# Performance work log

Measured on AMD Instinct MI355X. Metric: run time of the kernel, lower is better.

Reference implementation:

```python
import jax, jax.numpy as jnp
from jax import lax
import numpy as np

D = 128      # embedding_dim == GRU input_size == hidden_size
B, S, L = 256, 32, 32  # users, slates per user, slate length


def setup_inputs() -> dict:
    key = jax.random.key(0)
    ks = jax.random.split(key, 8)
    sc = 1.0 / np.sqrt(D)  # PyTorch GRU/Linear init scale
    return {
        "item_embs": jax.random.normal(ks[0], (B, S, L, D), jnp.float32),
        "user_embs": jax.random.normal(ks[1], (B, S, D), jnp.float32),
        "W_ih": jax.random.normal(ks[2], (3 * D, D), jnp.float32) * sc,
        "W_hh": jax.random.normal(ks[3], (3 * D, D), jnp.float32) * sc,
        "b_ih": jax.random.normal(ks[4], (3 * D,), jnp.float32) * sc,
        "b_hh": jax.random.normal(ks[5], (3 * D,), jnp.float32) * sc,
        "W_out": jax.random.normal(ks[6], (1, D), jnp.float32) * sc,
        "b_out": jax.random.normal(ks[7], (1,), jnp.float32) * sc,
    }


def reference(item_embs, user_embs, W_ih, W_hh, b_ih, b_hh, W_out, b_out):
    b, s, l, d = item_embs.shape
    x = item_embs.reshape(b * s, l, d)          # [N, L, D]
    h0 = user_embs.reshape(b * s, d)            # [N, D] initial hidden per slate

    # Precompute input-side gate projections for all timesteps (one big GEMM).
    gx = jnp.einsum('nld,gd->nlg', x, W_ih) + b_ih  # [N, L, 3D], PyTorch gate order r,z,n

    def step(h, gx_t):
        gh = h @ W_hh.T + b_hh                   # [N, 3D]
        xr, xz, xn = jnp.split(gx_t, 3, axis=-1)
        hr, hz, hn = jnp.split(gh, 3, axis=-1)
        r = jax.nn.sigmoid(xr + hr)
        z = jax.nn.sigmoid(xz + hz)
        n = jnp.tanh(xn + r * hn)
        h_new = (1.0 - z) * n + z * h
        return h_new, h_new

    _, hs = lax.scan(step, h0, jnp.swapaxes(gx, 0, 1))  # hs: [L, N, D]
    rnn_out = jnp.swapaxes(hs, 0, 1)             # [N, L, D]
    out = rnn_out @ W_out.T + b_out              # [N, L, 1]
    return out.reshape(b, s, l)
```

## Files before the change

kernel.cpp:

```cpp
#include <hip/hip_runtime.h>
#include <math.h>

#define DD   128
#define LL   32
#define MS   32
#define NT   1024
#define NSEQ 8192
#define XP   136
#define GP   36
#define OLP  36

#define GX_ELEMS   (384 * GP)
#define SMEM_XH_X  (2 * 384 * GP * 4)
#define SMEM_XH_H  (SMEM_XH_X + 2 * MS * XP * 2)
#define SMEM_OUTL  (SMEM_XH_H + 2 * MS * XP * 2)
#define SMEM_WOFL  (SMEM_OUTL + MS * OLP * 4)
#define SMEM_TOTAL (SMEM_WOFL + 4 * 64 * 8 * 2)

typedef short bf16x8 __attribute__((ext_vector_type(8)));
typedef float f32x4  __attribute__((ext_vector_type(4)));

#define MFMA __builtin_amdgcn_mfma_f32_16x16x32_bf16

__device__ __forceinline__ unsigned short f2bf(float f) {
    unsigned u = __float_as_uint(f);
    u += 0x7fffu + ((u >> 16) & 1u);
    return (unsigned short)(u >> 16);
}

#if __has_builtin(__builtin_amdgcn_cvt_pk_bf16_f32)
typedef __bf16 bf16x2_t __attribute__((ext_vector_type(2)));
__device__ __forceinline__ unsigned pack2(float a, float b) {
    union { bf16x2_t v; unsigned u; } c;
    c.v = __builtin_amdgcn_cvt_pk_bf16_f32(a, b);
    return c.u;
}
#else
__device__ __forceinline__ unsigned pack2(float a, float b) {
    return (unsigned)f2bf(a) | ((unsigned)f2bf(b) << 16);
}
#endif

__device__ __forceinline__ void pack8(float4 a, float4 b, unsigned short* dst) {
    union { unsigned u[4]; bf16x8 v; } pk;
    pk.u[0] = pack2(a.x, a.y); pk.u[1] = pack2(a.z, a.w);
    pk.u[2] = pack2(b.x, b.y); pk.u[3] = pack2(b.z, b.w);
    *(bf16x8*)dst = pk.v;
}

__device__ __forceinline__ float fast_rcp(float x) {
    return __builtin_amdgcn_rcpf(x);
}

__global__ void prep_weights(const float* __restrict__ Wih,
                             const float* __restrict__ Whh,
                             unsigned short* __restrict__ Wfrag) {
    int idx  = blockIdx.x * blockDim.x + threadIdx.x;
    int j    = idx & 7;
    int lane = (idx >> 3) & 63;
    int kk   = (idx >> 9) & 3;
    int sl   = (idx >> 11) & 7;
    int sg   = idx >> 14;
    int n = lane & 15, q = lane >> 4;
    int k  = kk * 32 + q * 8 + j;
    int g  = (sg >= 3) ? sg - 3 : sg;
    int gd = g * 128 + sl * 16 + n;
    const float* src = (sg >= 3) ? Whh : Wih;
    Wfrag[idx] = f2bf(src[gd * 128 + k]);
}

__global__ __launch_bounds__(NT, 4) void gru_mfma(
    const float* __restrict__ x,
    const float* __restrict__ h0,
    const unsigned short* __restrict__ Wfrag,
    const float* __restrict__ b_ih,
    const float* __restrict__ b_hh,
    const float* __restrict__ w_out,
    const float* __restrict__ b_out,
    float* __restrict__ out)
{
    extern __shared__ char smem[];
    float*          gxs  = (float*)(smem);
    unsigned short* xhx  = (unsigned short*)(smem + SMEM_XH_X);
    unsigned short* xhh  = (unsigned short*)(smem + SMEM_XH_H);
    float*          outl = (float*)(smem + SMEM_OUTL);
    unsigned short* wofl = (unsigned short*)(smem + SMEM_WOFL);

    const int tid  = threadIdx.x;
    const int n0   = blockIdx.x * MS;
    const int wv   = tid >> 6;
    const int lane = tid & 63;
    const int ln   = lane & 15;
    const int q    = lane >> 4;
    const bf16x8* W = (const bf16x8*)Wfrag;

    if (wv < 8) {
        const int d = wv * 16 + ln;
        const float bhr = b_hh[d], bhz = b_hh[DD + d], bhn = b_hh[2*DD + d];

        bf16x8 whr[4], whz[4], whn[4];
        #pragma unroll
        for (int kk = 0; kk < 4; ++kk) {
            whr[kk] = W[((24 + wv)*4 + kk)*64 + lane];
            whz[kk] = W[((32 + wv)*4 + kk)*64 + lane];
            whn[kk] = W[((40 + wv)*4 + kk)*64 + lane];
        }

        #pragma unroll
        for (int e = 0; e < 4; ++e) {
            int idx = tid * 4 + e;
            int j   = idx & 7;
            int l2  = (idx >> 3) & 63;
            int kk  = idx >> 9;
            int n2 = l2 & 15, q2 = l2 >> 4;
            wofl[idx] = (n2 == 0) ? f2bf(w_out[kk * 32 + q2 * 8 + j])
                                  : (unsigned short)0;
        }
        {
            const int gn = tid >> 4, gd8 = (tid & 15) * 8;
            const float* hb = h0 + (size_t)(n0 + gn) * DD + gd8;
            pack8(*(const float4*)hb, *(const float4*)(hb + 4),
                  &xhh[gn * XP + gd8]);
        }
        float hprev[8];
        #pragma unroll
        for (int tl = 0; tl < 2; ++tl)
            #pragma unroll
            for (int i = 0; i < 4; ++i)
                hprev[tl*4+i] = h0[(size_t)(n0 + tl*16 + q*4 + i) * DD + d];

        __syncthreads();
        __syncthreads();

        for (int t = 0; t < LL; ++t) {
            const int sl_ = t & 1;
            const float* gr = gxs + sl_ * GX_ELEMS;
            f32x4 cr[2], cz[2], ch[2];
            #pragma unroll
            for (int tl = 0; tl < 2; ++tl) {
                const int co = tl*16 + q*4;
                cr[tl] = *(const f32x4*)&gr[(d)*GP + co];
                cz[tl] = *(const f32x4*)&gr[(DD + d)*GP + co];
                ch[tl] = (f32x4){0.f, 0.f, 0.f, 0.f};
            }
            const unsigned short* hr0 = &xhh[sl_*MS*XP + ln*XP];
            const unsigned short* hr1 = hr0 + 16*XP;
            #pragma unroll
            for (int kk = 0; kk < 4; ++kk) {
                bf16x8 a0 = *(const bf16x8*)(hr0 + kk*32 + q*8);
                bf16x8 a1 = *(const bf16x8*)(hr1 + kk*32 + q*8);
                cr[0] = MFMA(a0, whr[kk], cr[0], 0,0,0);
                cr[1] = MFMA(a1, whr[kk], cr[1], 0,0,0);
                cz[0] = MFMA(a0, whz[kk], cz[0], 0,0,0);
                cz[1] = MFMA(a1, whz[kk], cz[1], 0,0,0);
                ch[0] = MFMA(a0, whn[kk], ch[0], 0,0,0);
                ch[1] = MFMA(a1, whn[kk], ch[1], 0,0,0);
            }
            f32x4 gnx[2];
            #pragma unroll
            for (int tl = 0; tl < 2; ++tl)
                gnx[tl] = *(const f32x4*)&gr[(2*DD + d)*GP + tl*16 + q*4];

            unsigned short* hw = xhh + (sl_ ^ 1)*MS*XP;
            #pragma unroll
            for (int tl = 0; tl < 2; ++tl)
                #pragma unroll
                for (int i = 0; i < 4; ++i) {
                    const float rr = fast_rcp(1.f + __expf(-(cr[tl][i] + bhr)));
                    const float zz = fast_rcp(1.f + __expf(-(cz[tl][i] + bhz)));
                    const float aa = gnx[tl][i] + rr * (ch[tl][i] + bhn);
                    const float ee = __expf(-2.f * aa);
                    const float th = 2.f * fast_rcp(1.f + ee) - 1.f;
                    const float hh = th + zz * (hprev[tl*4+i] - th);
                    hprev[tl*4+i] = hh;
                    hw[(tl*16 + q*4 + i)*XP + d] = f2bf(hh);
                }
            __syncthreads();
        }
        __syncthreads();

        if (tid < 256) {
            const int row = tid >> 3;
            const int t4  = (tid & 7) * 4;
            float4 v = *(const float4*)&outl[row * OLP + t4];
            *(float4*)(out + (size_t)(n0 + row) * LL + t4) = v;
        }
    } else {
        const int pv = wv - 8;
        const int dp = pv * 16 + ln;
        const float bir  = b_ih[dp];
        const float biz  = b_ih[DD + dp];
        const float bin_ = b_ih[2*DD + dp];
        const float bo   = b_out[0];

        bf16x8 wxr[4], wxz[4], wxn[4];
        #pragma unroll
        for (int kk = 0; kk < 4; ++kk) {
            wxr[kk] = W[((0  + pv)*4 + kk)*64 + lane];
            wxz[kk] = W[((8  + pv)*4 + kk)*64 + lane];
            wxn[kk] = W[((16 + pv)*4 + kk)*64 + lane];
        }

        const int pt  = tid & 511;
        const int gn  = pt >> 4;
        const int gd8 = (pt & 15) * 8;
        const float* xbase = x + ((size_t)(n0 + gn) * LL) * DD + gd8;

        pack8(*(const float4*)(xbase), *(const float4*)(xbase + 4),
              &xhx[gn * XP + gd8]);
        pack8(*(const float4*)(xbase + DD), *(const float4*)(xbase + DD + 4),
              &xhx[MS*XP + gn * XP + gd8]);

        __syncthreads();

        {
            const unsigned short* xr0 = &xhx[ln * XP];
            const unsigned short* xr1 = xr0 + 16*XP;
            f32x4 ar[2], az[2], an[2];
            #pragma unroll
            for (int tl = 0; tl < 2; ++tl) {
                ar[tl] = (f32x4){bir, bir, bir, bir};
                az[tl] = (f32x4){biz, biz, biz, biz};
                an[tl] = (f32x4){bin_, bin_, bin_, bin_};
            }
            #pragma unroll
            for (int kk = 0; kk < 4; ++kk) {
                bf16x8 a0 = *(const bf16x8*)(xr0 + kk*32 + q*8);
                bf16x8 a1 = *(const bf16x8*)(xr1 + kk*32 + q*8);
                ar[0] = MFMA(a0, wxr[kk], ar[0], 0,0,0);
                ar[1] = MFMA(a1, wxr[kk], ar[1], 0,0,0);
                az[0] = MFMA(a0, wxz[kk], az[0], 0,0,0);
                az[1] = MFMA(a1, wxz[kk], az[1], 0,0,0);
                an[0] = MFMA(a0, wxn[kk], an[0], 0,0,0);
                an[1] = MFMA(a1, wxn[kk], an[1], 0,0,0);
            }
            #pragma unroll
            for (int tl = 0; tl < 2; ++tl) {
                const int co = tl*16 + q*4;
                *(f32x4*)&gxs[(dp)*GP + co]        = ar[tl];
                *(f32x4*)&gxs[(DD + dp)*GP + co]   = az[tl];
                *(f32x4*)&gxs[(2*DD + dp)*GP + co] = an[tl];
            }
        }
        __syncthreads();

        for (int t = 0; t < LL; ++t) {
            float4 sa, sb;
            const int ts = t + 2;
            if (ts < LL) {
                sa = *(const float4*)(xbase + (size_t)ts * DD);
                sb = *(const float4*)(xbase + (size_t)ts * DD + 4);
            }
            if (t + 1 < LL) {
                const int sr = (t + 1) & 1;
                const unsigned short* xr0 = &xhx[sr*MS*XP + ln * XP];
                const unsigned short* xr1 = xr0 + 16*XP;
                f32x4 ar[2], az[2], an[2];
                #pragma unroll
                for (int tl = 0; tl < 2; ++tl) {
                    ar[tl] = (f32x4){bir, bir, bir, bir};
                    az[tl] = (f32x4){biz, biz, biz, biz};
                    an[tl] = (f32x4){bin_, bin_, bin_, bin_};
                }
                #pragma unroll
                for (int kk = 0; kk < 4; ++kk) {
                    bf16x8 a0 = *(const bf16x8*)(xr0 + kk*32 + q*8);
                    bf16x8 a1 = *(const bf16x8*)(xr1 + kk*32 + q*8);
                    ar[0] = MFMA(a0, wxr[kk], ar[0], 0,0,0);
                    ar[1] = MFMA(a1, wxr[kk], ar[1], 0,0,0);
                    az[0] = MFMA(a0, wxz[kk], az[0], 0,0,0);
                    az[1] = MFMA(a1, wxz[kk], az[1], 0,0,0);
                    an[0] = MFMA(a0, wxn[kk], an[0], 0,0,0);
                    an[1] = MFMA(a1, wxn[kk], an[1], 0,0,0);
                }
                float* gw = gxs + sr * GX_ELEMS;
                #pragma unroll
                for (int tl = 0; tl < 2; ++tl) {
                    const int co = tl*16 + q*4;
                    *(f32x4*)&gw[(dp)*GP + co]        = ar[tl];
                    *(f32x4*)&gw[(DD + dp)*GP + co]   = az[tl];
                    *(f32x4*)&gw[(2*DD + dp)*GP + co] = an[tl];
                }
            }
            if (pv < 2 && t >= 1) {
                f32x4 c4 = (f32x4){bo, bo, bo, bo};
                const unsigned short* hrw = &xhh[(t & 1)*MS*XP + (pv*16 + ln)*XP];
                #pragma unroll
                for (int kk = 0; kk < 4; ++kk) {
                    bf16x8 a = *(const bf16x8*)(hrw + kk*32 + q*8);
                    bf16x8 b = *(const bf16x8*)&wofl[(kk*64 + lane)*8];
                    c4 = MFMA(a, b, c4, 0,0,0);
                }
                if (ln == 0) {
                    #pragma unroll
                    for (int i = 0; i < 4; ++i)
                        outl[(pv*16 + q*4 + i)*OLP + (t - 1)] = c4[i];
                }
            }
            if (ts < LL)
                pack8(sa, sb, &xhx[(t & 1)*MS*XP + gn * XP + gd8]);

            __syncthreads();
        }

        if (pv < 2) {
            f32x4 c4 = (f32x4){bo, bo, bo, bo};
            const unsigned short* hrw = &xhh[(pv*16 + ln)*XP];
            #pragma unroll
            for (int kk = 0; kk < 4; ++kk) {
                bf16x8 a = *(const bf16x8*)(hrw + kk*32 + q*8);
                bf16x8 b = *(const bf16x8*)&wofl[(kk*64 + lane)*8];
                c4 = MFMA(a, b, c4, 0,0,0);
            }
            if (ln == 0) {
                #pragma unroll
                for (int i = 0; i < 4; ++i)
                    outl[(pv*16 + q*4 + i)*OLP + (LL - 1)] = c4[i];
            }
        }
        __syncthreads();
    }
}

extern "C" void kernel_launch(void* const* d_in, const int* in_sizes, int n_in,
                              void* d_out, int out_size, void* d_ws, size_t ws_size,
                              hipStream_t stream) {
    const float* item  = (const float*)d_in[0];
    const float* user  = (const float*)d_in[1];
    const float* W_ih  = (const float*)d_in[2];
    const float* W_hh  = (const float*)d_in[3];
    const float* b_ih  = (const float*)d_in[4];
    const float* b_hh  = (const float*)d_in[5];
    const float* W_out = (const float*)d_in[6];
    const float* b_out = (const float*)d_in[7];
    float* out = (float*)d_out;

    unsigned short* Wfrag = (unsigned short*)d_ws;

    static bool smem_cfg = false;
    if (!smem_cfg) {
        hipFuncSetAttribute((const void*)gru_mfma,
                            hipFuncAttributeMaxDynamicSharedMemorySize,
                            SMEM_TOTAL);
        smem_cfg = true;
    }

    prep_weights<<<384, 256, 0, stream>>>(W_ih, W_hh, Wfrag);
    gru_mfma<<<NSEQ / MS, NT, SMEM_TOTAL, stream>>>(item, user, Wfrag,
                                                    b_ih, b_hh, W_out, b_out, out);
}
```

Measured before the change: 222.2 us.

## Transpose MFMA operands and store gate projections in fragment-native LDS layout

Swaps the MFMA A/B operands so the weight fragment is the A operand and the hidden state the B operand. Each lane therefore owns four consecutive hidden dimensions for one sequence. The input-projection gates are stored to LDS in the exact per-lane fragment order and read back as contiguous f32x4, which removes the strided padded-row layout. The hidden-state writeback becomes one packed 8-byte store per 4 elements instead of four scalar bf16 stores. The r/z biases are pre-folded into the input-side accumulators, and s_setprio is raised around the recurrent MFMA block. LDS size changes, and correctness depends on the new fragment indexing and the output-row mapping matching.

After: 219.6 us. No clear change (-1.2%).

```diff
diff --git a/kernel.cpp b/kernel.cpp
--- a/kernel.cpp
+++ b/kernel.cpp
@@ -7,11 +7,11 @@
 #define NT   1024
 #define NSEQ 8192
 #define XP   136
-#define GP   36
 #define OLP  36
 
-#define GX_ELEMS   (384 * GP)
-#define SMEM_XH_X  (2 * 384 * GP * 4)
+#define NFRAG      48
+#define FRAGF      (NFRAG * 64 * 4)
+#define SMEM_XH_X  (2 * FRAGF * 4)
 #define SMEM_XH_H  (SMEM_XH_X + 2 * MS * XP * 2)
 #define SMEM_OUTL  (SMEM_XH_H + 2 * MS * XP * 2)
 #define SMEM_WOFL  (SMEM_OUTL + MS * OLP * 4)
@@ -80,7 +80,7 @@
     float* __restrict__ out)
 {
     extern __shared__ char smem[];
-    float*          gxs  = (float*)(smem);
+    float*          gxf  = (float*)(smem);
     unsigned short* xhx  = (unsigned short*)(smem + SMEM_XH_X);
     unsigned short* xhh  = (unsigned short*)(smem + SMEM_XH_H);
     float*          outl = (float*)(smem + SMEM_OUTL);
@@ -95,8 +95,8 @@
     const bf16x8* W = (const bf16x8*)Wfrag;
 
     if (wv < 8) {
-        const int d = wv * 16 + ln;
-        const float bhr = b_hh[d], bhz = b_hh[DD + d], bhn = b_hh[2*DD + d];
+        const int d4 = wv * 16 + q * 4;
+        const f32x4 bhn4 = *(const f32x4*)&b_hh[2*DD + d4];
 
         bf16x8 whr[4], whz[4], whn[4];
         #pragma unroll
@@ -122,59 +122,64 @@
             pack8(*(const float4*)hb, *(const float4*)(hb + 4),
                   &xhh[gn * XP + gd8]);
         }
-        float hprev[8];
-        #pragma unroll
-        for (int tl = 0; tl < 2; ++tl)
-            #pragma unroll
-            for (int i = 0; i < 4; ++i)
-                hprev[tl*4+i] = h0[(size_t)(n0 + tl*16 + q*4 + i) * DD + d];
+        float4 hp0 = *(const float4*)&h0[(size_t)(n0 + ln) * DD + d4];
+        float4 hp1 = *(const float4*)&h0[(size_t)(n0 + 16 + ln) * DD + d4];
+        float hprev[8] = {hp0.x, hp0.y, hp0.z, hp0.w,
+                          hp1.x, hp1.y, hp1.z, hp1.w};
 
         __syncthreads();
         __syncthreads();
 
         for (int t = 0; t < LL; ++t) {
             const int sl_ = t & 1;
-            const float* gr = gxs + sl_ * GX_ELEMS;
+            const float* gf = gxf + sl_ * FRAGF;
             f32x4 cr[2], cz[2], ch[2];
             #pragma unroll
-            for (int tl = 0; tl < 2; ++tl) {
-                const int co = tl*16 + q*4;
-                cr[tl] = *(const f32x4*)&gr[(d)*GP + co];
-                cz[tl] = *(const f32x4*)&gr[(DD + d)*GP + co];
-                ch[tl] = (f32x4){0.f, 0.f, 0.f, 0.f};
-            }
-            const unsigned short* hr0 = &xhh[sl_*MS*XP + ln*XP];
+            for (int st = 0; st < 2; ++st) {
+                cr[st] = *(const f32x4*)&gf[(((0*8 + wv)*2 + st)*64 + lane)*4];
+                cz[st] = *(const f32x4*)&gf[(((1*8 + wv)*2 + st)*64 + lane)*4];
+                ch[st] = (f32x4){0.f, 0.f, 0.f, 0.f};
+            }
+            const unsigned short* hr0 = xhh + sl_*MS*XP + ln*XP;
             const unsigned short* hr1 = hr0 + 16*XP;
+            __builtin_amdgcn_s_setprio(1);
             #pragma unroll
             for (int kk = 0; kk < 4; ++kk) {
-                bf16x8 a0 = *(const bf16x8*)(hr0 + kk*32 + q*8);
-                bf16x8 a1 = *(const bf16x8*)(hr1 + kk*32 + q*8);
-                cr[0] = MFMA(a0, whr[kk], cr[0], 0,0,0);
-                cr[1] = MFMA(a1, whr[kk], cr[1], 0,0,0);
-                cz[0] = MFMA(a0, whz[kk], cz[0], 0,0,0);
-                cz[1] = MFMA(a1, whz[kk], cz[1], 0,0,0);
-                ch[0] = MFMA(a0, whn[kk], ch[0], 0,0,0);
-                ch[1] = MFMA(a1, whn[kk], ch[1], 0,0,0);
-            }
+                bf16x8 b0 = *(const bf16x8*)(hr0 + kk*32 + q*8);
+                bf16x8 b1 = *(const bf16x8*)(hr1 + kk*32 + q*8);
+                cr[0] = MFMA(whr[kk], b0, cr[0], 0,0,0);
+                cr[1] = MFMA(whr[kk], b1, cr[1], 0,0,0);
+                cz[0] = MFMA(whz[kk], b0, cz[0], 0,0,0);
+                cz[1] = MFMA(whz[kk], b1, cz[1], 0,0,0);
+                ch[0] = MFMA(whn[kk], b0, ch[0], 0,0,0);
+                ch[1] = MFMA(whn[kk], b1, ch[1], 0,0,0);
+            }
+            __builtin_amdgcn_s_setprio(0);
             f32x4 gnx[2];
             #pragma unroll
-            for (int tl = 0; tl < 2; ++tl)
-                gnx[tl] = *(const f32x4*)&gr[(2*DD + d)*GP + tl*16 + q*4];
+            for (int st = 0; st < 2; ++st)
+                gnx[st] = *(const f32x4*)&gf[(((2*8 + wv)*2 + st)*64 + lane)*4];
 
             unsigned short* hw = xhh + (sl_ ^ 1)*MS*XP;
             #pragma unroll
-            for (int tl = 0; tl < 2; ++tl)
+            for (int st = 0; st < 2; ++st) {
+                float hh_[4];
                 #pragma unroll
                 for (int i = 0; i < 4; ++i) {
-                    const float rr = fast_rcp(1.f + __expf(-(cr[tl][i] + bhr)));
-                    const float zz = fast_rcp(1.f + __expf(-(cz[tl][i] + bhz)));
-                    const float aa = gnx[tl][i] + rr * (ch[tl][i] + bhn);
+                    const float rr = fast_rcp(1.f + __expf(-cr[st][i]));
+                    const float zz = fast_rcp(1.f + __expf(-cz[st][i]));
+                    const float aa = gnx[st][i] + rr * (ch[st][i] + bhn4[i]);
                     const float ee = __expf(-2.f * aa);
                     const float th = 2.f * fast_rcp(1.f + ee) - 1.f;
-                    const float hh = th + zz * (hprev[tl*4+i] - th);
-                    hprev[tl*4+i] = hh;
-                    hw[(tl*16 + q*4 + i)*XP + d] = f2bf(hh);
+                    const float hh = th + zz * (hprev[st*4+i] - th);
+                    hprev[st*4+i] = hh;
+                    hh_[i] = hh;
                 }
+                union { unsigned u[2]; unsigned long long ull; } hv;
+                hv.u[0] = pack2(hh_[0], hh_[1]);
+                hv.u[1] = pack2(hh_[2], hh_[3]);
+                *(unsigned long long*)&hw[(st*16 + ln)*XP + d4] = hv.ull;
+            }
             __syncthreads();
         }
         __syncthreads();
@@ -187,11 +192,18 @@
         }
     } else {
         const int pv = wv - 8;
-        const int dp = pv * 16 + ln;
-        const float bir  = b_ih[dp];
-        const float biz  = b_ih[DD + dp];
-        const float bin_ = b_ih[2*DD + dp];
-        const float bo   = b_out[0];
+        const int d4 = pv * 16 + q * 4;
+        f32x4 br4, bz4, bn4;
+        {
+            f32x4 a0 = *(const f32x4*)&b_ih[d4];
+            f32x4 a1 = *(const f32x4*)&b_hh[d4];
+            br4 = a0 + a1;
+            a0 = *(const f32x4*)&b_ih[DD + d4];
+            a1 = *(const f32x4*)&b_hh[DD + d4];
+            bz4 = a0 + a1;
+            bn4 = *(const f32x4*)&b_ih[2*DD + d4];
+        }
+        const float bo = b_out[0];
 
         bf16x8 wxr[4], wxz[4], wxn[4];
         #pragma unroll
@@ -213,35 +225,36 @@
 
         __syncthreads();
 
-        {
-            const unsigned short* xr0 = &xhx[ln * XP];
-            const unsigned short* xr1 = xr0 + 16*XP;
-            f32x4 ar[2], az[2], an[2];
-            #pragma unroll
-            for (int tl = 0; tl < 2; ++tl) {
-                ar[tl] = (f32x4){bir, bir, bir, bir};
-                az[tl] = (f32x4){biz, biz, biz, biz};
-                an[tl] = (f32x4){bin_, bin_, bin_, bin_};
-            }
-            #pragma unroll
-            for (int kk = 0; kk < 4; ++kk) {
-                bf16x8 a0 = *(const bf16x8*)(xr0 + kk*32 + q*8);
-                bf16x8 a1 = *(const bf16x8*)(xr1 + kk*32 + q*8);
-                ar[0] = MFMA(a0, wxr[kk], ar[0], 0,0,0);
-                ar[1] = MFMA(a1, wxr[kk], ar[1], 0,0,0);
-                az[0] = MFMA(a0, wxz[kk], az[0], 0,0,0);
-                az[1] = MFMA(a1, wxz[kk], az[1], 0,0,0);
-                an[0] = MFMA(a0, wxn[kk], an[0], 0,0,0);
-                an[1] = MFMA(a1, wxn[kk], an[1], 0,0,0);
-            }
-            #pragma unroll
-            for (int tl = 0; tl < 2; ++tl) {
-                const int co = tl*16 + q*4;
-                *(f32x4*)&gxs[(dp)*GP + co]        = ar[tl];
-                *(f32x4*)&gxs[(DD + dp)*GP + co]   = az[tl];
-                *(f32x4*)&gxs[(2*DD + dp)*GP + co] = an[tl];
-            }
-        }
+#define GX_STEP(TT)                                                            \
+        {                                                                      \
+            const int sr = (TT) & 1;                                           \
+            const unsigned short* xr0 = xhx + sr*MS*XP + ln*XP;                \
+            const unsigned short* xr1 = xr0 + 16*XP;                           \
+            f32x4 ar[2], az[2], an[2];                                         \
+            ar[0] = br4; ar[1] = br4;                                          \
+            az[0] = bz4; az[1] = bz4;                                          \
+            an[0] = bn4; an[1] = bn4;                                          \
+            _Pragma("unroll")                                                  \
+            for (int kk = 0; kk < 4; ++kk) {                                   \
+                bf16x8 b0 = *(const bf16x8*)(xr0 + kk*32 + q*8);               \
+                bf16x8 b1 = *(const bf16x8*)(xr1 + kk*32 + q*8);               \
+                ar[0] = MFMA(wxr[kk], b0, ar[0], 0,0,0);                       \
+                ar[1] = MFMA(wxr[kk], b1, ar[1], 0,0,0);                       \
+                az[0] = MFMA(wxz[kk], b0, az[0], 0,0,0);                       \
+                az[1] = MFMA(wxz[kk], b1, az[1], 0,0,0);                       \
+                an[0] = MFMA(wxn[kk], b0, an[0], 0,0,0);                       \
+                an[1] = MFMA(wxn[kk], b1, an[1], 0,0,0);                       \
+            }                                                                  \
+            float* gw = gxf + sr * FRAGF;                                      \
+            _Pragma("unroll")                                                  \
+            for (int st = 0; st < 2; ++st) {                                   \
+                *(f32x4*)&gw[(((0*8 + pv)*2 + st)*64 + lane)*4] = ar[st];      \
+                *(f32x4*)&gw[(((1*8 + pv)*2 + st)*64 + lane)*4] = az[st];      \
+                *(f32x4*)&gw[(((2*8 + pv)*2 + st)*64 + lane)*4] = an[st];      \
+            }                                                                  \
+        }
+
+        GX_STEP(0)
         __syncthreads();
 
         for (int t = 0; t < LL; ++t) {
@@ -251,51 +264,19 @@
                 sa = *(const float4*)(xbase + (size_t)ts * DD);
                 sb = *(const float4*)(xbase + (size_t)ts * DD + 4);
             }
-            if (t + 1 < LL) {
-                const int sr = (t + 1) & 1;
-                const unsigned short* xr0 = &xhx[sr*MS*XP + ln * XP];
-                const unsigned short* xr1 = xr0 + 16*XP;
-                f32x4 ar[2], az[2], an[2];
-                #pragma unroll
-                for (int tl = 0; tl < 2; ++tl) {
-                    ar[tl] = (f32x4){bir, bir, bir, bir};
-                    az[tl] = (f32x4){biz, biz, biz, biz};
-                    an[tl] = (f32x4){bin_, bin_, bin_, bin_};
-                }
+            if (t + 1 < LL) GX_STEP(t + 1)
+
+            if (pv < 2 && t >= 1) {
+                f32x4 c4 = (f32x4){bo, bo, bo, bo};
+                const unsigned short* hrw = xhh + (t & 1)*MS*XP + (pv*16 + ln)*XP;
                 #pragma unroll
                 for (int kk = 0; kk < 4; ++kk) {
-                    bf16x8 a0 = *(const bf16x8*)(xr0 + kk*32 + q*8);
-                    bf16x8 a1 = *(const bf16x8*)(xr1 + kk*32 + q*8);
-                    ar[0] = MFMA(a0, wxr[kk], ar[0], 0,0,0);
-                    ar[1] = MFMA(a1, wxr[kk], ar[1], 0,0,0);
-                    az[0] = MFMA(a0, wxz[kk], az[0], 0,0,0);
-                    az[1] = MFMA(a1, wxz[kk], az[1], 0,0,0);
-                    an[0] = MFMA(a0, wxn[kk], an[0], 0,0,0);
-                    an[1] = MFMA(a1, wxn[kk], an[1], 0,0,0);
-                }
-                float* gw = gxs + sr * GX_ELEMS;
-                #pragma unroll
-                for (int tl = 0; tl < 2; ++tl) {
-                    const int co = tl*16 + q*4;
-                    *(f32x4*)&gw[(dp)*GP + co]        = ar[tl];
-                    *(f32x4*)&gw[(DD + dp)*GP + co]   = az[tl];
-                    *(f32x4*)&gw[(2*DD + dp)*GP + co] = an[tl];
-                }
-            }
-            if (pv < 2 && t >= 1) {
-                f32x4 c4 = (f32x4){bo, bo, bo, bo};
-                const unsigned short* hrw = &xhh[(t & 1)*MS*XP + (pv*16 + ln)*XP];
-                #pragma unroll
-                for (int kk = 0; kk < 4; ++kk) {
-                    bf16x8 a = *(const bf16x8*)(hrw + kk*32 + q*8);
-                    bf16x8 b = *(const bf16x8*)&wofl[(kk*64 + lane)*8];
+                    bf16x8 a = *(const bf16x8*)&wofl[(kk*64 + lane)*8];
+                    bf16x8 b = *(const bf16x8*)(hrw + kk*32 + q*8);
                     c4 = MFMA(a, b, c4, 0,0,0);
                 }
-                if (ln == 0) {
-                    #pragma unroll
-                    for (int i = 0; i < 4; ++i)
-                        outl[(pv*16 + q*4 + i)*OLP + (t - 1)] = c4[i];
-                }
+                if (q == 0)
+                    outl[(pv*16 + ln)*OLP + (t - 1)] = c4[0];
             }
             if (ts < LL)
                 pack8(sa, sb, &xhx[(t & 1)*MS*XP + gn * XP + gd8]);
@@ -305,20 +286,18 @@
 
         if (pv < 2) {
             f32x4 c4 = (f32x4){bo, bo, bo, bo};
-            const unsigned short* hrw = &xhh[(pv*16 + ln)*XP];
+            const unsigned short* hrw = xhh + (pv*16 + ln)*XP;
             #pragma unroll
             for (int kk = 0; kk < 4; ++kk) {
-                bf16x8 a = *(const bf16x8*)(hrw + kk*32 + q*8);
-                bf16x8 b = *(const bf16x8*)&wofl[(kk*64 + lane)*8];
+                bf16x8 a = *(const bf16x8*)&wofl[(kk*64 + lane)*8];
+                bf16x8 b = *(const bf16x8*)(hrw + kk*32 + q*8);
                 c4 = MFMA(a, b, c4, 0,0,0);
             }
-            if (ln == 0) {
-                #pragma unroll
-                for (int i = 0; i < 4; ++i)
-                    outl[(pv*16 + q*4 + i)*OLP + (LL - 1)] = c4[i];
-            }
-        }
-        __syncthreads();
+            if (q == 0)
+                outl[(pv*16 + ln)*OLP + (LL - 1)] = c4[0];
+        }
+        __syncthreads();
+#undef GX_STEP
     }
 }
 
```
